# Performance work log

Measured on AMD Instinct MI355X. Metric: run time of the kernel, lower is better.

## Reference

```python
import jax, jax.numpy as jnp
import numpy as np

MODEL_DIM = 768
NUM_HEADS = 6
HEAD_DIM = 128
T = 4096
EPS = float(jnp.finfo(jnp.float32).eps)


def _rms_norm(x):
    # F.rms_norm(x, (x.size(-1),)) with no weight
    return x * jax.lax.rsqrt(jnp.mean(x * x, axis=-1, keepdims=True) + EPS)


def _rotary_tables(max_len, head_dim):
    # angular_freq: (1/1024)**linspace(0,1,dim//4) then pad dim//4 zeros -> half dim = dim//2
    nf = head_dim // 4
    af = (1.0 / 1024.0) ** jnp.linspace(0.0, 1.0, nf, dtype=jnp.float32)
    af = jnp.concatenate([af, jnp.zeros(nf, dtype=jnp.float32)])  # [head_dim//2]
    t = jnp.arange(max_len, dtype=jnp.float32)
    theta = jnp.einsum('i,j->ij', t, af)  # [max_len, head_dim//2]
    return jnp.cos(theta), jnp.sin(theta)


def _apply_rotary(x_bthd, pos_id, cos_tab, sin_tab):
    cos = cos_tab[pos_id][:, None, :]  # [T,1,hd/2] -> broadcast over heads
    sin = sin_tab[pos_id][:, None, :]
    x1, x2 = jnp.split(x_bthd.astype(jnp.float32), 2, axis=-1)
    y1 = x1 * cos + x2 * sin
    y2 = -x1 * sin + x2 * cos
    return jnp.concatenate([y1, y2], axis=-1).astype(x_bthd.dtype)


def setup_inputs() -> dict:
    key = jax.random.key(0)
    ks = jax.random.split(key, 8)
    bound = (3.0 ** 0.5) * 0.5 * MODEL_DIM ** (-0.5)  # CastedLinear init
    x = jax.random.normal(ks[0], (1, T, MODEL_DIM), dtype=jnp.float32)
    v_residual = jax.random.normal(ks[1], (1, T, NUM_HEADS, HEAD_DIM), dtype=jnp.float32)
    pos_id = jnp.arange(T, dtype=jnp.int32)
    mask = jnp.tril(jnp.ones((T, T), dtype=bool))  # causal block_mask equivalent
    Wq = jax.random.uniform(ks[2], (MODEL_DIM, MODEL_DIM), jnp.float32, -bound, bound)
    Wk = jax.random.uniform(ks[3], (MODEL_DIM, MODEL_DIM), jnp.float32, -bound, bound)
    Wv = jax.random.uniform(ks[4], (MODEL_DIM, MODEL_DIM), jnp.float32, -bound, bound)
    Wo = jax.random.uniform(ks[5], (MODEL_DIM, MODEL_DIM), jnp.float32, -bound, bound)
    lamb = jnp.float32(0.5)
    return {"x": x, "v_residual": v_residual, "Wq": Wq, "Wk": Wk, "Wv": Wv,
            "Wo": Wo, "lamb": lamb, "pos_id": pos_id, "mask": mask}


def reference(x, v_residual, Wq, Wk, Wv, Wo, lamb, pos_id, mask):
    B, Tn, _ = x.shape
    cos_tab, sin_tab = _rotary_tables(Tn, HEAD_DIM)
    # QKV projections (F.linear: x @ W.T)
    q = (x @ Wq.T).reshape(B, Tn, NUM_HEADS, HEAD_DIM)
    k = (x @ Wk.T).reshape(B, Tn, NUM_HEADS, HEAD_DIM)
    v = (x @ Wv.T).reshape(B, Tn, NUM_HEADS, HEAD_DIM)
    q = _apply_rotary(_rms_norm(q), pos_id, cos_tab, sin_tab)
    k = _apply_rotary(_rms_norm(k), pos_id, cos_tab, sin_tab)
    # value-residual mixing
    v = (1.0 - lamb) * v + lamb * v_residual
    # attention with block mask (scale = 1/sqrt(head_dim), flex_attention default)
    scale = 1.0 / (HEAD_DIM ** 0.5)
    scores = jnp.einsum('bthd,bshd->bhts', q, k) * scale  # [B,H,T,T]
    scores = jnp.where(mask[None, None, :, :], scores, -jnp.inf)
    attn = jax.nn.softmax(scores, axis=-1)
    y = jnp.einsum('bhts,bshd->bthd', attn, v).reshape(B, Tn, NUM_HEADS * HEAD_DIM)
    return (y @ Wo.T, v_residual)
```

## Files before the change

kernel.cpp:

```cpp
#include <hip/hip_runtime.h>
#include <hip/hip_bf16.h>

typedef unsigned short u16;
typedef __attribute__((ext_vector_type(8))) short short8;
typedef __attribute__((ext_vector_type(4))) float f32x4;
typedef __attribute__((ext_vector_type(16))) float f32x16;
typedef __attribute__((ext_vector_type(2))) unsigned int u32x2;

#define MODEL 768
#define SCALE2 0.1275174137f

__device__ __forceinline__ float bf2f(u16 u) {
  unsigned int x = ((unsigned int)u) << 16;
  return __uint_as_float(x);
}
__device__ __forceinline__ u16 f2bf(float f) {
  unsigned int x = __float_as_uint(f);
  unsigned int r = (x + 0x7FFFu + ((x >> 16) & 1u)) >> 16;
  return (u16)r;
}
__device__ __forceinline__ void lds_ld16(const u16* g, u16* l) {
  __builtin_amdgcn_global_load_lds((const __attribute__((address_space(1))) void*)g,
                                   (__attribute__((address_space(3))) void*)l, 16, 0, 0);
}
__device__ __forceinline__ unsigned int cvtpk_bf16(float lo, float hi_) {
  unsigned int r;
  asm("v_cvt_pk_bf16_f32 %0, %1, %2" : "=v"(r) : "v"(lo), "v"(hi_));
  return r;
}

__global__ __launch_bounds__(256) void r21_cvt(const float* __restrict__ x,
                                               const float* __restrict__ wq,
                                               const float* __restrict__ wk,
                                               const float* __restrict__ wv,
                                               u16* __restrict__ xb,
                                               u16* __restrict__ wqb,
                                               u16* __restrict__ wkb,
                                               u16* __restrict__ wvb) {
  int i = blockIdx.x * 256 + threadIdx.x;
  const float* src;
  u16* dst;
  int j;
  if (i < 786432) { src = x; dst = xb; j = i; }
  else if (i < 933888) { src = wq; dst = wqb; j = i - 786432; }
  else if (i < 1081344) { src = wk; dst = wkb; j = i - 933888; }
  else { src = wv; dst = wvb; j = i - 1081344; }
  float4 v = ((const float4*)src)[j];
  ushort4 o;
  o.x = f2bf(v.x); o.y = f2bf(v.y); o.z = f2bf(v.z); o.w = f2bf(v.w);
  ((ushort4*)dst)[j] = o;
}

__global__ __launch_bounds__(256) void r21_gemm_qkv(const u16* __restrict__ A,
                                                    const u16* __restrict__ W0,
                                                    const u16* __restrict__ W1,
                                                    const u16* __restrict__ W2,
                                                    u16* __restrict__ C0,
                                                    u16* __restrict__ C1,
                                                    u16* __restrict__ C2) {
  const u16* Wb = (blockIdx.z == 0) ? W0 : (blockIdx.z == 1) ? W1 : W2;
  u16* C = (blockIdx.z == 0) ? C0 : (blockIdx.z == 1) ? C1 : C2;
  __shared__ u16 As[64 * 32];
  __shared__ u16 Bs[128 * 32];
  const int tid = threadIdx.x;
  const int w = tid >> 6, l = tid & 63;
  const int lr = l & 15, lg = l >> 4;
  const int m0 = blockIdx.x * 64, n0 = blockIdx.y * 128;
  const int wr = (w >> 1) * 32, wc = (w & 1) * 64;
  const int sr = w * 16 + (l >> 2);
  const int sc = (l & 3) * 8;
  f32x4 acc[2][4] = {};
  for (int k0 = 0; k0 < 768; k0 += 32) {
    __syncthreads();
    lds_ld16(A + (size_t)(m0 + sr) * 768 + k0 + sc, As + w * 512);
#pragma unroll
    for (int i = 0; i < 2; i++) {
      int ii = w * 2 + i;
      int row = ii * 16 + (l >> 2);
      lds_ld16(Wb + (size_t)(n0 + row) * 768 + k0 + sc, Bs + ii * 512);
    }
    __syncthreads();
    short8 af[2], bfr[4];
#pragma unroll
    for (int mr = 0; mr < 2; mr++) af[mr] = *(const short8*)(As + (wr + mr * 16 + lr) * 32 + lg * 8);
#pragma unroll
    for (int nc = 0; nc < 4; nc++) bfr[nc] = *(const short8*)(Bs + (wc + nc * 16 + lr) * 32 + lg * 8);
#pragma unroll
    for (int mr = 0; mr < 2; mr++)
#pragma unroll
      for (int nc = 0; nc < 4; nc++)
        acc[mr][nc] = __builtin_amdgcn_mfma_f32_16x16x32_bf16(af[mr], bfr[nc], acc[mr][nc], 0, 0, 0);
  }
#pragma unroll
  for (int mr = 0; mr < 2; mr++)
#pragma unroll
    for (int nc = 0; nc < 4; nc++)
#pragma unroll
      for (int ri = 0; ri < 4; ri++) {
        int row = m0 + wr + mr * 16 + lg * 4 + ri;
        int col = n0 + wc + nc * 16 + lr;
        C[(size_t)row * 768 + col] = f2bf(acc[mr][nc][ri]);
      }
}

__global__ __launch_bounds__(256) void r21_gemm_proj(const float* __restrict__ accO,
                                                     const float* __restrict__ accL,
                                                     const u16* __restrict__ Wb,
                                                     float* __restrict__ C) {
  __shared__ u16 As[64 * 32];
  __shared__ u16 Bs[128 * 32];
  const int tid = threadIdx.x;
  const int w = tid >> 6, l = tid & 63;
  const int lr = l & 15, lg = l >> 4;
  const int m0 = blockIdx.x * 64, n0 = blockIdx.y * 128;
  const int wr = (w >> 1) * 32, wc = (w & 1) * 64;
  const int arow = tid >> 2;
  const int aoff = (tid & 3) * 8;
  const int sc = (l & 3) * 8;
  f32x4 acc[2][4] = {};
  for (int k0 = 0; k0 < 768; k0 += 32) {
    __syncthreads();
    {
      const float* ap = accO + (size_t)(m0 + arow) * 768 + k0 + aoff;
      float rl = 1.0f / accL[(m0 + arow) * 6 + (k0 >> 7)];
      u16* dp = As + arow * 32 + aoff;
      float4 f0 = ((const float4*)ap)[0];
      float4 f1 = ((const float4*)ap)[1];
      ushort4 b0, b1;
      b0.x = f2bf(f0.x * rl); b0.y = f2bf(f0.y * rl);
      b0.z = f2bf(f0.z * rl); b0.w = f2bf(f0.w * rl);
      b1.x = f2bf(f1.x * rl); b1.y = f2bf(f1.y * rl);
      b1.z = f2bf(f1.z * rl); b1.w = f2bf(f1.w * rl);
      *(ushort4*)(dp) = b0;
      *(ushort4*)(dp + 4) = b1;
    }
#pragma unroll
    for (int i = 0; i < 2; i++) {
      int ii = w * 2 + i;
      int row = ii * 16 + (l >> 2);
      lds_ld16(Wb + (size_t)(n0 + row) * 768 + k0 + sc, Bs + ii * 512);
    }
    __syncthreads();
    short8 af[2], bfr[4];
#pragma unroll
    for (int mr = 0; mr < 2; mr++) af[mr] = *(const short8*)(As + (wr + mr * 16 + lr) * 32 + lg * 8);
#pragma unroll
    for (int nc = 0; nc < 4; nc++) bfr[nc] = *(const short8*)(Bs + (wc + nc * 16 + lr) * 32 + lg * 8);
#pragma unroll
    for (int mr = 0; mr < 2; mr++)
#pragma unroll
      for (int nc = 0; nc < 4; nc++)
        acc[mr][nc] = __builtin_amdgcn_mfma_f32_16x16x32_bf16(af[mr], bfr[nc], acc[mr][nc], 0, 0, 0);
  }
#pragma unroll
  for (int mr = 0; mr < 2; mr++)
#pragma unroll
    for (int nc = 0; nc < 4; nc++)
#pragma unroll
      for (int ri = 0; ri < 4; ri++) {
        int row = m0 + wr + mr * 16 + lg * 4 + ri;
        int col = n0 + wc + nc * 16 + lr;
        C[(size_t)row * 768 + col] = acc[mr][nc][ri];
      }
}

__global__ __launch_bounds__(256) void r21_normrope(u16* __restrict__ qb,
                                                    u16* __restrict__ kb,
                                                    u16* __restrict__ vb,
                                                    const float* __restrict__ vres,
                                                    const float* __restrict__ lambp,
                                                    const int* __restrict__ pos,
                                                    float* __restrict__ out1,
                                                    float* __restrict__ accZ,
                                                    const float* __restrict__ wo,
                                                    u16* __restrict__ wob) {
  {
    int gid = blockIdx.x * 256 + threadIdx.x;
    if (gid < 792576) {
      float4 z = {0.0f, 0.0f, 0.0f, 0.0f};
      ((float4*)accZ)[gid] = z;
    } else if (gid < 792576 + 147456) {
      int j = gid - 792576;
      float4 v = ((const float4*)wo)[j];
      ushort4 o;
      o.x = f2bf(v.x); o.y = f2bf(v.y); o.z = f2bf(v.z); o.w = f2bf(v.w);
      ((ushort4*)wob)[j] = o;
    }
  }
  const int wg = blockIdx.x * 4 + (threadIdx.x >> 6);
  const int l = threadIdx.x & 63;
  const int t = wg / 6;
  const int h = wg - t * 6;
  const size_t base = (size_t)t * MODEL + h * 128;
  const float EPS = 1.1920928955078125e-07f;

  float c = 1.0f, sn = 0.0f;
  if (l < 32) {
    float af = exp2f(-10.0f * (float)l * (1.0f / 31.0f));
    float th = (float)pos[t] * af;
    sincosf(th, &sn, &c);
  }
  {
    float a = bf2f(qb[base + l]), b = bf2f(qb[base + 64 + l]);
    float ss = a * a + b * b;
#pragma unroll
    for (int off = 32; off; off >>= 1) ss += __shfl_xor(ss, off);
    float r = rsqrtf(ss * (1.0f / 128.0f) + EPS);
    float an = a * r, bn = b * r;
    qb[base + l] = f2bf(an * c + bn * sn);
    qb[base + 64 + l] = f2bf(bn * c - an * sn);
  }
  {
    float a = bf2f(kb[base + l]), b = bf2f(kb[base + 64 + l]);
    float ss = a * a + b * b;
#pragma unroll
    for (int off = 32; off; off >>= 1) ss += __shfl_xor(ss, off);
    float r = rsqrtf(ss * (1.0f / 128.0f) + EPS);
    float an = a * r, bn = b * r;
    kb[base + l] = f2bf(an * c + bn * sn);
    kb[base + 64 + l] = f2bf(bn * c - an * sn);
  }
  {
    float lm = *lambp;
    float a = bf2f(vb[base + l]), b = bf2f(vb[base + 64 + l]);
    float ra = vres[base + l], rb = vres[base + 64 + l];
    vb[base + l] = f2bf((1.0f - lm) * a + lm * ra);
    vb[base + 64 + l] = f2bf((1.0f - lm) * b + lm * rb);
    out1[base + l] = ra;
    out1[base + 64 + l] = rb;
  }
}

__global__ __launch_bounds__(128, 2) void r21_attn(const u16* __restrict__ Q,
                                                   const u16* __restrict__ K,
                                                   const u16* __restrict__ V,
                                                   float* __restrict__ accO,
                                                   float* __restrict__ accL) {
  const int bx = blockIdx.x;
  const int h = bx / 160;
  const int u = 159 - (bx - h * 160);
  int qt, kc;
  if (u < 16)      { qt = u;                      kc = 0; }
  else if (u < 48) { int v = u - 16; qt = 16 + (v >> 1); kc = v & 1; }
  else if (u < 96) { int v = u - 48; int q3 = v / 3; qt = 32 + q3; kc = v - 3 * q3; }
  else             { int v = u - 96; qt = 48 + (v >> 2); kc = v & 3; }
  const int rowmax = 64 * qt + 63;
  const int c0 = kc << 10;
  const bool islast = (c0 + 1024 > rowmax);
  const int cend = islast ? (rowmax + 1) : (c0 + 1024);
  const int niter = (cend - c0) >> 6;

  const int tid = threadIdx.x;
  const int wv = tid >> 6, l = tid & 63;
  const int lq = l & 31;
  const int hi = l >> 5;

  __shared__ u16 Ks[64][128];
  __shared__ u16 vt[128][72];

  const int c_ = tid & 31, cc = c_ * 4, g = tid >> 5;
  const int vswz = (c_ & 7) << 3;

  const int qr = qt * 64 + wv * 32;
  const int qrow = qr + lq;

  short8 qf[8];
  {
    const u16* qp = Q + (size_t)qrow * 768 + h * 128 + hi * 8;
#pragma unroll
    for (int s = 0; s < 8; s++) qf[s] = *(const short8*)(qp + s * 16);
  }
  f32x16 oacc[4] = {};
  float lsum = 0.0f;

  for (int kv = 0; kv < niter; kv++) {
    const int k0 = c0 + kv * 64;

#pragma unroll
    for (int i = 0; i < 8; i++) {
      int rbase = wv * 32 + i * 4;
      int row = rbase + (l >> 4);
      int blk = (l & 15) ^ (row & 7);
      lds_ld16(K + (size_t)(k0 + row) * 768 + h * 128 + blk * 8, &Ks[rbase][0]);
    }
#pragma unroll
    for (int it = 0; it < 8; it++) {
      int rloc = 2 * (g + 4 * it);
      ushort4 va = *(const ushort4*)(V + (size_t)(k0 + rloc) * 768 + h * 128 + cc);
      ushort4 vb = *(const ushort4*)(V + (size_t)(k0 + rloc + 1) * 768 + h * 128 + cc);
      int rs = rloc ^ vswz;
      u16 a0[4] = {va.x, va.y, va.z, va.w};
      u16 b0[4] = {vb.x, vb.y, vb.z, vb.w};
#pragma unroll
      for (int q = 0; q < 4; q++) {
        ushort2 t2; t2.x = a0[q]; t2.y = b0[q];
        *(ushort2*)&vt[cc + q][rs] = t2;
      }
    }
    __syncthreads();

    f32x16 sac0 = {}, sac1 = {};
    __builtin_amdgcn_s_setprio(1);
    {
      const int r0_ = lq, r1_ = 32 + lq;
#pragma unroll
      for (int s = 0; s < 8; s++) {
        short8 kf0 = *(const short8*)(&Ks[r0_][((s * 2 + hi) ^ (r0_ & 7)) * 8]);
        sac0 = __builtin_amdgcn_mfma_f32_32x32x16_bf16(kf0, qf[s], sac0, 0, 0, 0);
      }
#pragma unroll
      for (int s = 0; s < 8; s++) {
        short8 kf1 = *(const short8*)(&Ks[r1_][((s * 2 + hi) ^ (r1_ & 7)) * 8]);
        sac1 = __builtin_amdgcn_mfma_f32_32x32x16_bf16(kf1, qf[s], sac1, 0, 0, 0);
      }
    }
    __builtin_amdgcn_s_setprio(0);

    float p[32];
    const bool maskit = islast && (kv == niter - 1);
    if (maskit) {
#pragma unroll
      for (int r = 0; r < 16; r++) {
        int kvg = k0 + (r & 3) + 8 * (r >> 2) + 4 * hi;
        p[r] = (kvg <= qrow) ? exp2f(sac0[r] * SCALE2) : 0.0f;
      }
#pragma unroll
      for (int r = 0; r < 16; r++) {
        int kvg = k0 + 32 + (r & 3) + 8 * (r >> 2) + 4 * hi;
        p[16 + r] = (kvg <= qrow) ? exp2f(sac1[r] * SCALE2) : 0.0f;
      }
    } else {
#pragma unroll
      for (int r = 0; r < 16; r++) p[r] = exp2f(sac0[r] * SCALE2);
#pragma unroll
      for (int r = 0; r < 16; r++) p[16 + r] = exp2f(sac1[r] * SCALE2);
    }
#pragma unroll
    for (int i = 0; i < 32; i++) lsum += p[i];

    union { unsigned int w[4]; short8 v; } pa[4];
#pragma unroll
    for (int s = 0; s < 4; s++) {
      const int b = s * 8;
      unsigned int cA0 = cvtpk_bf16(p[b + 0], p[b + 1]);
      unsigned int cA1 = cvtpk_bf16(p[b + 2], p[b + 3]);
      unsigned int cB0 = cvtpk_bf16(p[b + 4], p[b + 5]);
      unsigned int cB1 = cvtpk_bf16(p[b + 6], p[b + 7]);
      u32x2 s0 = __builtin_amdgcn_permlane32_swap(cA0, cB0, false, false);
      u32x2 s1 = __builtin_amdgcn_permlane32_swap(cA1, cB1, false, false);
      pa[s].w[0] = s0[0]; pa[s].w[1] = s1[0]; pa[s].w[2] = s0[1]; pa[s].w[3] = s1[1];
    }

    __builtin_amdgcn_s_setprio(1);
#pragma unroll
    for (int dt = 0; dt < 4; dt++) {
      const int d = dt * 32 + lq;
      const int dz = ((d >> 2) & 7) << 3;
#pragma unroll
      for (int s = 0; s < 4; s++) {
        short8 vf = *(const short8*)(&vt[d][(s * 16 + hi * 8) ^ dz]);
        oacc[dt] = __builtin_amdgcn_mfma_f32_32x32x16_bf16(pa[s].v, vf, oacc[dt], 0, 0, 0);
      }
    }
    __builtin_amdgcn_s_setprio(0);
    __syncthreads();
  }

#pragma unroll
  for (int dt = 0; dt < 4; dt++) {
    const int d = dt * 32 + lq;
#pragma unroll
    for (int r = 0; r < 16; r++) {
      int qrw = qr + (r & 3) + 8 * (r >> 2) + 4 * hi;
      unsafeAtomicAdd(&accO[(size_t)qrw * 768 + h * 128 + d], oacc[dt][r]);
    }
  }
  unsafeAtomicAdd(&accL[qrow * 6 + h], lsum);
}

extern "C" void kernel_launch(void* const* d_in, const int* in_sizes, int n_in,
                              void* d_out, int out_size, void* d_ws, size_t ws_size,
                              hipStream_t stream) {
  const float* x = (const float*)d_in[0];
  const float* vres = (const float*)d_in[1];
  const float* Wq = (const float*)d_in[2];
  const float* Wk = (const float*)d_in[3];
  const float* Wv = (const float*)d_in[4];
  const float* Wo = (const float*)d_in[5];
  const float* lamb = (const float*)d_in[6];
  const int* pos = (const int*)d_in[7];
  float* out = (float*)d_out;

  u16* xb = (u16*)d_ws;
  u16* qb = xb + 3145728;
  u16* kb = qb + 3145728;
  u16* vb = kb + 3145728;
  float* accO = (float*)((char*)d_ws + 25165824);
  float* accL = accO + 3145728;
  u16* wqb = (u16*)accO;
  u16* wkb = wqb + 589824;
  u16* wvb = wkb + 589824;
  u16* wob = xb;
  float* out1 = out + 3145728;

  r21_cvt<<<4800, 256, 0, stream>>>(x, Wq, Wk, Wv, xb, wqb, wkb, wvb);
  r21_gemm_qkv<<<dim3(64, 6, 3), 256, 0, stream>>>(xb, wqb, wkb, wvb, qb, kb, vb);
  r21_normrope<<<6144, 256, 0, stream>>>(qb, kb, vb, vres, lamb, pos, out1,
                                         accO, Wo, wob);
  r21_attn<<<960, 128, 0, stream>>>(qb, kb, vb, accO, accL);
  r21_gemm_proj<<<dim3(64, 6), 256, 0, stream>>>(accO, accL, wob, out);
}
```

Measured before the change: 141.0 us.

## Fold softmax scale into Q, compute row sums via MFMA, widen V transpose

Folds the attention scale into the Q normalization so the attention loop no longer multiplies each score before exp2. The scalar per-lane accumulation of probability sums is replaced by an MFMA against a vector of bf16 ones, with row sums atomically added per row at the end. The V transpose into LDS now loads four rows per step and writes ushort4 instead of ushort2, cutting LDS store count. Risks include bf16-rounded probabilities in the row sum, extra MFMA work per tile, and rounding Q after scaling.

```diff
diff --git a/kernel.cpp b/kernel.cpp
--- a/kernel.cpp
+++ b/kernel.cpp
@@ -29,7 +29,7 @@
   return r;
 }
 
-__global__ __launch_bounds__(256) void r21_cvt(const float* __restrict__ x,
+__global__ __launch_bounds__(256) void r22_cvt(const float* __restrict__ x,
                                                const float* __restrict__ wq,
                                                const float* __restrict__ wk,
                                                const float* __restrict__ wv,
@@ -51,7 +51,7 @@
   ((ushort4*)dst)[j] = o;
 }
 
-__global__ __launch_bounds__(256) void r21_gemm_qkv(const u16* __restrict__ A,
+__global__ __launch_bounds__(256) void r22_gemm_qkv(const u16* __restrict__ A,
                                                     const u16* __restrict__ W0,
                                                     const u16* __restrict__ W1,
                                                     const u16* __restrict__ W2,
@@ -103,7 +103,7 @@
       }
 }
 
-__global__ __launch_bounds__(256) void r21_gemm_proj(const float* __restrict__ accO,
+__global__ __launch_bounds__(256) void r22_gemm_proj(const float* __restrict__ accO,
                                                      const float* __restrict__ accL,
                                                      const u16* __restrict__ Wb,
                                                      float* __restrict__ C) {
@@ -164,7 +164,7 @@
       }
 }
 
-__global__ __launch_bounds__(256) void r21_normrope(u16* __restrict__ qb,
+__global__ __launch_bounds__(256) void r22_normrope(u16* __restrict__ qb,
                                                     u16* __restrict__ kb,
                                                     u16* __restrict__ vb,
                                                     const float* __restrict__ vres,
@@ -205,7 +205,7 @@
     float ss = a * a + b * b;
 #pragma unroll
     for (int off = 32; off; off >>= 1) ss += __shfl_xor(ss, off);
-    float r = rsqrtf(ss * (1.0f / 128.0f) + EPS);
+    float r = rsqrtf(ss * (1.0f / 128.0f) + EPS) * SCALE2;
     float an = a * r, bn = b * r;
     qb[base + l] = f2bf(an * c + bn * sn);
     qb[base + 64 + l] = f2bf(bn * c - an * sn);
@@ -231,7 +231,7 @@
   }
 }
 
-__global__ __launch_bounds__(128, 2) void r21_attn(const u16* __restrict__ Q,
+__global__ __launch_bounds__(128, 2) void r22_attn(const u16* __restrict__ Q,
                                                    const u16* __restrict__ K,
                                                    const u16* __restrict__ V,
                                                    float* __restrict__ accO,
@@ -264,6 +264,10 @@
   const int qr = qt * 64 + wv * 32;
   const int qrow = qr + lq;
 
+  short8 ones;
+#pragma unroll
+  for (int i = 0; i < 8; i++) ones[i] = (short)0x3F80;
+
   short8 qf[8];
   {
     const u16* qp = Q + (size_t)qrow * 768 + h * 128 + hi * 8;
@@ -271,7 +275,7 @@
     for (int s = 0; s < 8; s++) qf[s] = *(const short8*)(qp + s * 16);
   }
   f32x16 oacc[4] = {};
-  float lsum = 0.0f;
+  f32x16 lacc = {};
 
   for (int kv = 0; kv < niter; kv++) {
     const int k0 = c0 + kv * 64;
@@ -284,18 +288,24 @@
       lds_ld16(K + (size_t)(k0 + row) * 768 + h * 128 + blk * 8, &Ks[rbase][0]);
     }
 #pragma unroll
-    for (int it = 0; it < 8; it++) {
-      int rloc = 2 * (g + 4 * it);
-      ushort4 va = *(const ushort4*)(V + (size_t)(k0 + rloc) * 768 + h * 128 + cc);
-      ushort4 vb = *(const ushort4*)(V + (size_t)(k0 + rloc + 1) * 768 + h * 128 + cc);
-      int rs = rloc ^ vswz;
-      u16 a0[4] = {va.x, va.y, va.z, va.w};
-      u16 b0[4] = {vb.x, vb.y, vb.z, vb.w};
-#pragma unroll
-      for (int q = 0; q < 4; q++) {
-        ushort2 t2; t2.x = a0[q]; t2.y = b0[q];
-        *(ushort2*)&vt[cc + q][rs] = t2;
-      }
+    for (int it = 0; it < 4; it++) {
+      int quad = g + 4 * it;
+      int r0 = 4 * quad;
+      const u16* vp = V + (size_t)(k0 + r0) * 768 + h * 128 + cc;
+      ushort4 v0 = *(const ushort4*)(vp);
+      ushort4 v1 = *(const ushort4*)(vp + 768);
+      ushort4 v2 = *(const ushort4*)(vp + 1536);
+      ushort4 v3 = *(const ushort4*)(vp + 2304);
+      int rs4 = r0 ^ vswz;
+      ushort4 t4;
+      t4.x = v0.x; t4.y = v1.x; t4.z = v2.x; t4.w = v3.x;
+      *(ushort4*)&vt[cc + 0][rs4] = t4;
+      t4.x = v0.y; t4.y = v1.y; t4.z = v2.y; t4.w = v3.y;
+      *(ushort4*)&vt[cc + 1][rs4] = t4;
+      t4.x = v0.z; t4.y = v1.z; t4.z = v2.z; t4.w = v3.z;
+      *(ushort4*)&vt[cc + 2][rs4] = t4;
+      t4.x = v0.w; t4.y = v1.w; t4.z = v2.w; t4.w = v3.w;
+      *(ushort4*)&vt[cc + 3][rs4] = t4;
     }
     __syncthreads();
 
@@ -322,21 +332,19 @@
 #pragma unroll
       for (int r = 0; r < 16; r++) {
         int kvg = k0 + (r & 3) + 8 * (r >> 2) + 4 * hi;
-        p[r] = (kvg <= qrow) ? exp2f(sac0[r] * SCALE2) : 0.0f;
+        p[r] = (kvg <= qrow) ? exp2f(sac0[r]) : 0.0f;
       }
 #pragma unroll
       for (int r = 0; r < 16; r++) {
         int kvg = k0 + 32 + (r & 3) + 8 * (r >> 2) + 4 * hi;
-        p[16 + r] = (kvg <= qrow) ? exp2f(sac1[r] * SCALE2) : 0.0f;
+        p[16 + r] = (kvg <= qrow) ? exp2f(sac1[r]) : 0.0f;
       }
     } else {
 #pragma unroll
-      for (int r = 0; r < 16; r++) p[r] = exp2f(sac0[r] * SCALE2);
-#pragma unroll
-      for (int r = 0; r < 16; r++) p[16 + r] = exp2f(sac1[r] * SCALE2);
-    }
-#pragma unroll
-    for (int i = 0; i < 32; i++) lsum += p[i];
+      for (int r = 0; r < 16; r++) p[r] = exp2f(sac0[r]);
+#pragma unroll
+      for (int r = 0; r < 16; r++) p[16 + r] = exp2f(sac1[r]);
+    }
 
     union { unsigned int w[4]; short8 v; } pa[4];
 #pragma unroll
@@ -353,6 +361,9 @@
 
     __builtin_amdgcn_s_setprio(1);
 #pragma unroll
+    for (int s = 0; s < 4; s++)
+      lacc = __builtin_amdgcn_mfma_f32_32x32x16_bf16(pa[s].v, ones, lacc, 0, 0, 0);
+#pragma unroll
     for (int dt = 0; dt < 4; dt++) {
       const int d = dt * 32 + lq;
       const int dz = ((d >> 2) & 7) << 3;
@@ -375,7 +386,13 @@
       unsafeAtomicAdd(&accO[(size_t)qrw * 768 + h * 128 + d], oacc[dt][r]);
     }
   }
-  unsafeAtomicAdd(&accL[qrow * 6 + h], lsum);
+  if (lq == 0) {
+#pragma unroll
+    for (int r = 0; r < 16; r++) {
+      int qrw = qr + (r & 3) + 8 * (r >> 2) + 4 * hi;
+      unsafeAtomicAdd(&accL[qrw * 6 + h], lacc[r]);
+    }
+  }
 }
 
 extern "C" void kernel_launch(void* const* d_in, const int* in_sizes, int n_in,
@@ -403,10 +420,10 @@
   u16* wob = xb;
   float* out1 = out + 3145728;
 
-  r21_cvt<<<4800, 256, 0, stream>>>(x, Wq, Wk, Wv, xb, wqb, wkb, wvb);
-  r21_gemm_qkv<<<dim3(64, 6, 3), 256, 0, stream>>>(xb, wqb, wkb, wvb, qb, kb, vb);
-  r21_normrope<<<6144, 256, 0, stream>>>(qb, kb, vb, vres, lamb, pos, out1,
+  r22_cvt<<<4800, 256, 0, stream>>>(x, Wq, Wk, Wv, xb, wqb, wkb, wvb);
+  r22_gemm_qkv<<<dim3(64, 6, 3), 256, 0, stream>>>(xb, wqb, wkb, wvb, qb, kb, vb);
+  r22_normrope<<<6144, 256, 0, stream>>>(qb, kb, vb, vres, lamb, pos, out1,
                                          accO, Wo, wob);
-  r21_attn<<<960, 128, 0, stream>>>(qb, kb, vb, accO, accL);
-  r21_gemm_proj<<<dim3(64, 6), 256, 0, stream>>>(accO, accL, wob, out);
-}
+  r22_attn<<<960, 128, 0, stream>>>(qb, kb, vb, accO, accL);
+  r22_gemm_proj<<<dim3(64, 6), 256, 0, stream>>>(accO, accL, wob, out);
+}
```

Result: no change. 140.6 us (-0.3%).
